# Kernel tuning notes

Measured on AMD Instinct MI355X. Metric: run time of the kernel, lower is better.

Reference implementation:

```python
import jax, jax.numpy as jnp
import numpy as np

N_NODES = 100000


def gcn_conv(x, edge_index, W, b, n_nodes):
    """PyG GCNConv: h = x @ W; add self-loops; symmetric deg norm; sum-aggregate; + bias."""
    src, dst = edge_index[0], edge_index[1]
    loop = jnp.arange(n_nodes, dtype=src.dtype)
    src = jnp.concatenate([src, loop])  # [E + N]
    dst = jnp.concatenate([dst, loop])
    w = jnp.ones(src.shape[0], dtype=x.dtype)  # edge_weight=None -> ones
    deg = jax.ops.segment_sum(w, dst, num_segments=n_nodes)  # in-degree incl. self-loop
    dinv = jnp.where(deg > 0, jax.lax.rsqrt(deg), 0.0).astype(x.dtype)
    norm = dinv[src] * w * dinv[dst]  # [E + N]
    h = x @ W  # [N, d_out] transform first (PyG order)
    msgs = norm[:, None] * h[src]  # [E + N, d_out] gathered, normalized messages
    out = jax.ops.segment_sum(msgs, dst, num_segments=n_nodes)
    return out + b


def setup_inputs() -> dict:
    key = jax.random.key(0)
    k1, k2, k3, k4 = jax.random.split(key, 4)
    d_in, d_hid, d_out = 128, 128, 64
    E = 3200000
    x = jax.random.normal(k1, (N_NODES, d_in), dtype=jnp.float32)
    edge_index = jax.random.randint(k2, (2, E), 0, N_NODES, dtype=jnp.int64)
    W1 = jax.random.normal(k3, (d_in, d_hid), dtype=jnp.float32) / np.sqrt(d_in)
    b1 = jnp.zeros((d_hid,), dtype=jnp.float32)
    W2 = jax.random.normal(k4, (d_hid, d_out), dtype=jnp.float32) / np.sqrt(d_hid)
    b2 = jnp.zeros((d_out,), dtype=jnp.float32)
    return {"x": x, "edge_index": edge_index, "W1": W1, "b1": b1, "W2": W2, "b2": b2}


def reference(x, edge_index, W1, b1, W2, b2):
    h = gcn_conv(x, edge_index, W1, b1, N_NODES)
    h = jax.nn.relu(h)
    out = gcn_conv(h, edge_index, W2, b2, N_NODES)
    return out
```

## Files before the change

### kernel.cpp

```cpp
#include <hip/hip_runtime.h>


#define N_NODES 100000
#define NBLK  512
#define NBUCK 391

typedef __attribute__((ext_vector_type(8))) short short8;
typedef __attribute__((ext_vector_type(4))) float f32x4;

__device__ __forceinline__ unsigned short f2bf(float f) {
    union { float f; unsigned u; } c; c.f = f;
    unsigned r = (c.u + 0x7fffu + ((c.u >> 16) & 1u)) >> 16;
    return (unsigned short)r;
}
__device__ __forceinline__ float2 bfpair(unsigned u) {
    union { float f; unsigned u; } a, b;
    a.u = u << 16; b.u = u & 0xffff0000u;
    return make_float2(a.f, b.f);
}
__device__ __forceinline__ unsigned packbf(float a, float b) {
    return (unsigned)f2bf(a) | ((unsigned)f2bf(b) << 16);
}

__global__ void detect64_k(const unsigned long long* __restrict__ ei, int* __restrict__ flag) {
    unsigned long long v = ei[threadIdx.x & 63];
    unsigned long long bad = __ballot(v >= (1ULL << 32));
    if (threadIdx.x == 0) *flag = (bad == 0ULL) ? 1 : 0;
}

__device__ __forceinline__ int edge_at(const void* ei, int is64, long long idx) {
    if (is64) return (int)((const long long*)ei)[idx];
    return ((const int*)ei)[idx];
}

__global__ __launch_bounds__(256) void count1_k(const void* __restrict__ ei,
                                                const int* __restrict__ flag,
                                                int* __restrict__ bhist, int E) {
    __shared__ int lh[NBUCK];
    int t = threadIdx.x;
    for (int i = t; i < NBUCK; i += 256) lh[i] = 0;
    __syncthreads();
    int is64 = *flag;
    int C = (E + NBLK - 1) / NBLK;
    int lo = blockIdx.x * C;
    int hi = lo + C; if (hi > E) hi = E;
    for (int e = lo + t; e < hi; e += 256) {
        int d = edge_at(ei, is64, (long long)E + e);
        if ((unsigned)d < (unsigned)N_NODES) atomicAdd(&lh[d >> 8], 1);
    }
    __syncthreads();
    for (int i = t; i < NBUCK; i += 256) bhist[(size_t)i * NBLK + blockIdx.x] = lh[i];
}

__global__ void scan1_k(const int* __restrict__ cnt, int* __restrict__ partial,
                        int* __restrict__ bsum, int n) {
    __shared__ int sm[256];
    int t = threadIdx.x;
    int base = blockIdx.x * 1024 + t * 4;
    int v[4]; int loc = 0;
#pragma unroll
    for (int j = 0; j < 4; ++j) { v[j] = (base + j < n) ? cnt[base + j] : 0; loc += v[j]; }
    sm[t] = loc; __syncthreads();
    for (int off = 1; off < 256; off <<= 1) {
        int x = (t >= off) ? sm[t - off] : 0;
        __syncthreads();
        sm[t] += x;
        __syncthreads();
    }
    int incl = sm[t];
    int run = incl - loc;
    if (t == 255) bsum[blockIdx.x] = incl;
#pragma unroll
    for (int j = 0; j < 4; ++j) {
        if (base + j < n) partial[base + j] = run;
        run += v[j];
    }
}

__global__ void scan2_k(int* __restrict__ bsum, int nb) {
    __shared__ int sm[256];
    int t = threadIdx.x;
    int v = (t < nb) ? bsum[t] : 0;
    sm[t] = v; __syncthreads();
    for (int off = 1; off < 256; off <<= 1) {
        int x = (t >= off) ? sm[t - off] : 0;
        __syncthreads();
        sm[t] += x;
        __syncthreads();
    }
    if (t < nb) bsum[t] = sm[t] - v;
}

__global__ void scanadd_k(const int* __restrict__ bsum, int* __restrict__ arr,
                          const int* __restrict__ raw, int* __restrict__ tot, int n) {
    int base = blockIdx.x * 1024 + threadIdx.x * 4;
    int add = bsum[blockIdx.x];
#pragma unroll
    for (int j = 0; j < 4; ++j) {
        int i = base + j;
        if (i < n) {
            int v = arr[i] + add;
            arr[i] = v;
            if (i == n - 1) *tot = v + raw[i];
        }
    }
}

__global__ void scan3_k(const int* __restrict__ bsum, const int* __restrict__ cnt,
                        int* __restrict__ row_ptr, float* __restrict__ dinv, int n) {
    int base = blockIdx.x * 1024 + threadIdx.x * 4;
    int add = bsum[blockIdx.x];
#pragma unroll
    for (int j = 0; j < 4; ++j) {
        int i = base + j;
        if (i < n) {
            row_ptr[i] += add;
            dinv[i] = rsqrtf((float)(cnt[i] + 1));
        }
    }
}

__global__ __launch_bounds__(256) void write1_k(const void* __restrict__ ei,
                                                const int* __restrict__ flag,
                                                const int* __restrict__ bbase,
                                                unsigned* __restrict__ pairs, int E) {
    __shared__ int lofs[NBUCK];
    int t = threadIdx.x;
    for (int i = t; i < NBUCK; i += 256) lofs[i] = bbase[(size_t)i * NBLK + blockIdx.x];
    __syncthreads();
    int is64 = *flag;
    int C = (E + NBLK - 1) / NBLK;
    int lo = blockIdx.x * C;
    int hi = lo + C; if (hi > E) hi = E;
    for (int e = lo + t; e < hi; e += 256) {
        int s = edge_at(ei, is64, e);
        int d = edge_at(ei, is64, (long long)E + e);
        if ((unsigned)d >= (unsigned)N_NODES) continue;
        if ((unsigned)s >= (unsigned)N_NODES) s = 0;
        int b = d >> 8;
        int p = atomicAdd(&lofs[b], 1);
        pairs[p] = (unsigned)s | ((unsigned)(d & 255) << 17);
    }
}

__global__ __launch_bounds__(256) void degree_k(const unsigned* __restrict__ pairs,
                                                const int* __restrict__ bbase,
                                                const int* __restrict__ tot,
                                                int* __restrict__ cnt, int Nn) {
    __shared__ int lh[256];
    int b = blockIdx.x;
    int t = threadIdx.x;
    lh[t] = 0;
    __syncthreads();
    int lo = bbase[(size_t)b * NBLK];
    int hi = (b == NBUCK - 1) ? *tot : bbase[((size_t)b + 1) * NBLK];
    for (int i = lo + t; i < hi; i += 256) {
        unsigned p = __builtin_nontemporal_load(pairs + i);
        atomicAdd(&lh[p >> 17], 1);
    }
    __syncthreads();
    int n0 = b << 8;
    if (n0 + t < Nn) cnt[n0 + t] = lh[t];
}

__global__ __launch_bounds__(256) void fill3_k(const unsigned* __restrict__ pairs,
                                               const int* __restrict__ bbase,
                                               const int* __restrict__ tot,
                                               const int* __restrict__ row_ptr,
                                               int* __restrict__ colv, int Nn) {
    __shared__ int cur[256];
    int b = blockIdx.x;
    int t = threadIdx.x;
    int n0 = b << 8;
    int nn = Nn - n0; if (nn > 256) nn = 256;
    if (t < nn) cur[t] = row_ptr[n0 + t];
    __syncthreads();
    int lo = bbase[(size_t)b * NBLK];
    int hi = (b == NBUCK - 1) ? *tot : bbase[((size_t)b + 1) * NBLK];
    for (int i = lo + t; i < hi; i += 256) {
        unsigned p = __builtin_nontemporal_load(pairs + i);
        int dl = (int)(p >> 17);
        int slot = atomicAdd(&cur[dl], 1);
        colv[slot] = (int)(p & 0x1FFFFu);
    }
}

__global__ void prep_w_k(const float* __restrict__ W1, const float* __restrict__ W2,
                         unsigned short* __restrict__ w1bf, unsigned short* __restrict__ w2bf) {
    int i = blockIdx.x * 256 + threadIdx.x;
    if (i < 128 * 128) { int k = i >> 7, f = i & 127; w1bf[f * 128 + k] = f2bf(W1[i]); }
    if (i < 128 * 64)  { int k = i >> 6, f = i & 63;  w2bf[f * 128 + k] = f2bf(W2[i]); }
}

__global__ __launch_bounds__(256) void gemm1_k(const float* __restrict__ x,
                                               const unsigned short* __restrict__ w1bf,
                                               unsigned* __restrict__ h1, int Nn) {
    __shared__ __align__(16) unsigned short sA[128][136];
    __shared__ __align__(16) unsigned short sB[64][136];
    int tid = threadIdx.x;
    int n0g = blockIdx.x * 64;
    {
        const uint4* src = (const uint4*)w1bf;
#pragma unroll
        for (int l = 0; l < 8; ++l) {
            int idx = tid + l * 256;
            int f = idx >> 4, kq = idx & 15;
            *(uint4*)&sA[f][kq * 8] = src[idx];
        }
    }
    {
        int n = tid >> 2, kq = tid & 3;
        int gn = n0g + n; if (gn >= Nn) gn = Nn - 1;
        const float4* xr = (const float4*)(x + (size_t)gn * 128 + kq * 32);
        unsigned short* dst = &sB[n][kq * 32];
#pragma unroll
        for (int i = 0; i < 8; ++i) {
            float4 v = xr[i];
            dst[i * 4 + 0] = f2bf(v.x); dst[i * 4 + 1] = f2bf(v.y);
            dst[i * 4 + 2] = f2bf(v.z); dst[i * 4 + 3] = f2bf(v.w);
        }
    }
    __syncthreads();
    int wave = tid >> 6, lane = tid & 63;
    int quad = lane >> 4, l16 = lane & 15;
    f32x4 z = {0.f, 0.f, 0.f, 0.f};
    f32x4 acc[8];
#pragma unroll
    for (int t = 0; t < 8; ++t) acc[t] = z;
#pragma unroll
    for (int kk = 0; kk < 4; ++kk) {
        int kb = kk * 32 + quad * 8;
        short8 a = *(const short8*)&sB[wave * 16 + l16][kb];
#pragma unroll
        for (int ft = 0; ft < 8; ++ft) {
            short8 b = *(const short8*)&sA[ft * 16 + l16][kb];
            acc[ft] = __builtin_amdgcn_mfma_f32_16x16x32_bf16(a, b, acc[ft], 0, 0, 0);
        }
    }
    __syncthreads();
    unsigned short (*sC)[136] = sA;
#pragma unroll
    for (int ft = 0; ft < 8; ++ft)
#pragma unroll
        for (int r = 0; r < 4; ++r)
            sC[wave * 16 + quad * 4 + r][ft * 16 + l16] = f2bf(acc[ft][r]);
    __syncthreads();
#pragma unroll
    for (int l = 0; l < 4; ++l) {
        int idx = tid + l * 256;
        int row = idx >> 4, q = idx & 15;
        int gn = n0g + row;
        if (gn < Nn)
            *(uint4*)&h1[(size_t)gn * 64 + q * 4] = *(uint4*)&sC[row][q * 8];
    }
}

__global__ __launch_bounds__(256) void gemm2_k(const unsigned* __restrict__ hr,
                                               const unsigned short* __restrict__ w2bf,
                                               unsigned* __restrict__ h2, int Nn) {
    __shared__ __align__(16) unsigned short sA[64][136];
    __shared__ __align__(16) unsigned short sB[64][136];
    int tid = threadIdx.x;
    int n0g = blockIdx.x * 64;
    {
        const uint4* src = (const uint4*)w2bf;
#pragma unroll
        for (int l = 0; l < 4; ++l) {
            int idx = tid + l * 256;
            int f = idx >> 4, kq = idx & 15;
            *(uint4*)&sA[f][kq * 8] = src[idx];
        }
    }
    {
        const uint4* src = (const uint4*)hr;
#pragma unroll
        for (int l = 0; l < 4; ++l) {
            int idx = tid + l * 256;
            int row = idx >> 4, q = idx & 15;
            int gn = n0g + row; if (gn >= Nn) gn = Nn - 1;
            *(uint4*)&sB[row][q * 8] = src[(size_t)gn * 16 + q];
        }
    }
    __syncthreads();
    int wave = tid >> 6, lane = tid & 63;
    int quad = lane >> 4, l16 = lane & 15;
    f32x4 z = {0.f, 0.f, 0.f, 0.f};
    f32x4 acc[4];
#pragma unroll
    for (int t = 0; t < 4; ++t) acc[t] = z;
#pragma unroll
    for (int kk = 0; kk < 4; ++kk) {
        int kb = kk * 32 + quad * 8;
        short8 a = *(const short8*)&sB[wave * 16 + l16][kb];
#pragma unroll
        for (int ft = 0; ft < 4; ++ft) {
            short8 b = *(const short8*)&sA[ft * 16 + l16][kb];
            acc[ft] = __builtin_amdgcn_mfma_f32_16x16x32_bf16(a, b, acc[ft], 0, 0, 0);
        }
    }
    __syncthreads();
    unsigned short (*sC)[136] = sA;
#pragma unroll
    for (int ft = 0; ft < 4; ++ft)
#pragma unroll
        for (int r = 0; r < 4; ++r)
            sC[wave * 16 + quad * 4 + r][ft * 16 + l16] = f2bf(acc[ft][r]);
    __syncthreads();
#pragma unroll
    for (int l = 0; l < 2; ++l) {
        int idx = tid + l * 256;
        int row = idx >> 3, q = idx & 7;
        int gn = n0g + row;
        if (gn < Nn)
            *(uint4*)&h2[(size_t)gn * 32 + q * 4] = *(uint4*)&sC[row][q * 8];
    }
}

__global__ __launch_bounds__(256) void agg1_k(const unsigned* __restrict__ h,
                                              const int* __restrict__ row_ptr,
                                              const int* __restrict__ cnt,
                                              const int* __restrict__ colv,
                                              const float* __restrict__ dinv,
                                              const float* __restrict__ bias,
                                              unsigned* __restrict__ out, int Nn, int E) {
    int node = blockIdx.x * 4 + (threadIdx.x >> 6);
    if (node >= Nn) return;
    int lane = threadIdx.x & 63;
    float di = dinv[node];
    int start = row_ptr[node];
    int deg = cnt[node];

    float2 hv = bfpair(h[(size_t)node * 64 + lane]);
    float w0 = di * di;
    float ax = w0 * hv.x, ay = w0 * hv.y;

    for (int base = 0; base < deg; base += 64) {
        int idx = base + lane;
        int ci = start + idx; if (ci >= E) ci = E - 1;
        int sl = colv[ci];
        float wl = (idx < deg) ? dinv[sl] : 0.f;
        int m = deg - base; if (m > 64) m = 64;
        int j = 0;
        for (; j + 4 <= m; j += 4) {
            int s0 = __shfl(sl, j),     s1 = __shfl(sl, j + 1);
            int s2 = __shfl(sl, j + 2), s3 = __shfl(sl, j + 3);
            float e0 = di * __shfl(wl, j),     e1 = di * __shfl(wl, j + 1);
            float e2 = di * __shfl(wl, j + 2), e3 = di * __shfl(wl, j + 3);
            unsigned u0 = h[(size_t)s0 * 64 + lane];
            unsigned u1 = h[(size_t)s1 * 64 + lane];
            unsigned u2 = h[(size_t)s2 * 64 + lane];
            unsigned u3 = h[(size_t)s3 * 64 + lane];
            float2 v0 = bfpair(u0), v1 = bfpair(u1), v2 = bfpair(u2), v3 = bfpair(u3);
            ax = fmaf(e0, v0.x, ax); ay = fmaf(e0, v0.y, ay);
            ax = fmaf(e1, v1.x, ax); ay = fmaf(e1, v1.y, ay);
            ax = fmaf(e2, v2.x, ax); ay = fmaf(e2, v2.y, ay);
            ax = fmaf(e3, v3.x, ax); ay = fmaf(e3, v3.y, ay);
        }
        for (; j < m; ++j) {
            int s = __shfl(sl, j);
            float we = di * __shfl(wl, j);
            float2 v = bfpair(h[(size_t)s * 64 + lane]);
            ax = fmaf(we, v.x, ax); ay = fmaf(we, v.y, ay);
        }
    }
    float r0 = fmaxf(ax + bias[lane * 2], 0.f);
    float r1 = fmaxf(ay + bias[lane * 2 + 1], 0.f);
    out[(size_t)node * 64 + lane] = packbf(r0, r1);
}

__global__ __launch_bounds__(256) void agg2_k(const unsigned* __restrict__ h,
                                              const int* __restrict__ row_ptr,
                                              const int* __restrict__ cnt,
                                              const int* __restrict__ colv,
                                              const float* __restrict__ dinv,
                                              const float* __restrict__ bias,
                                              float* __restrict__ out, int Nn, int E) {
    int node = blockIdx.x * 4 + (threadIdx.x >> 6);
    if (node >= Nn) return;
    int lane = threadIdx.x & 63;
    int half = lane >> 5, fp = lane & 31;
    float di = dinv[node];
    int start = row_ptr[node];
    int deg = cnt[node];

    float2 hv = bfpair(h[(size_t)node * 32 + fp]);
    float w0 = (half == 0) ? di * di : 0.f;
    float ax = w0 * hv.x, ay = w0 * hv.y;

    for (int base = 0; base < deg; base += 64) {
        int idx = base + lane;
        int ci = start + idx; if (ci >= E) ci = E - 1;
        int sl = colv[ci];
        float wl = (idx < deg) ? dinv[sl] : 0.f;
        int m = deg - base; if (m > 64) m = 64;
        int j = 0;
        for (; j + 8 <= m; j += 8) {
            int q0 = j + half, q1 = j + 2 + half, q2 = j + 4 + half, q3 = j + 6 + half;
            int s0 = __shfl(sl, q0), s1 = __shfl(sl, q1);
            int s2 = __shfl(sl, q2), s3 = __shfl(sl, q3);
            float e0 = di * __shfl(wl, q0), e1 = di * __shfl(wl, q1);
            float e2 = di * __shfl(wl, q2), e3 = di * __shfl(wl, q3);
            unsigned u0 = h[(size_t)s0 * 32 + fp];
            unsigned u1 = h[(size_t)s1 * 32 + fp];
            unsigned u2 = h[(size_t)s2 * 32 + fp];
            unsigned u3 = h[(size_t)s3 * 32 + fp];
            float2 v0 = bfpair(u0), v1 = bfpair(u1), v2 = bfpair(u2), v3 = bfpair(u3);
            ax = fmaf(e0, v0.x, ax); ay = fmaf(e0, v0.y, ay);
            ax = fmaf(e1, v1.x, ax); ay = fmaf(e1, v1.y, ay);
            ax = fmaf(e2, v2.x, ax); ay = fmaf(e2, v2.y, ay);
            ax = fmaf(e3, v3.x, ax); ay = fmaf(e3, v3.y, ay);
        }
        for (; j < m; j += 2) {
            int q = j + half;
            int s = __shfl(sl, q & 63);
            float we = di * __shfl(wl, q & 63);
            float2 v = bfpair(h[(size_t)s * 32 + fp]);
            ax = fmaf(we, v.x, ax); ay = fmaf(we, v.y, ay);
        }
    }
    ax += __shfl_xor(ax, 32, 64);
    ay += __shfl_xor(ay, 32, 64);
    if (half == 0) {
        float2 r = make_float2(ax + bias[fp * 2], ay + bias[fp * 2 + 1]);
        *(float2*)&out[(size_t)node * 64 + fp * 2] = r;
    }
}

extern "C" void kernel_launch(void* const* d_in, const int* in_sizes, int n_in,
                              void* d_out, int out_size, void* d_ws, size_t ws_size,
                              hipStream_t stream) {
    const float* x  = (const float*)d_in[0];
    const void*  ei = d_in[1];
    const float* W1 = (const float*)d_in[2];
    const float* b1 = (const float*)d_in[3];
    const float* W2 = (const float*)d_in[4];
    const float* b2 = (const float*)d_in[5];

    const int N = N_NODES;
    const int E = in_sizes[1] / 2;
    const int NB = NBLK * NBUCK;

    char* w = (char*)d_ws;
    size_t off = 0;
    auto take = [&](size_t bytes) {
        void* p = w + off;
        off = (off + bytes + 255) & ~(size_t)255;
        return p;
    };
    int*   flag    = (int*)take(2 * sizeof(int));
    int*   tot     = flag + 1;
    int*   cnt     = (int*)take((size_t)N * 4);
    int*   row_ptr = (int*)take((size_t)N * 4);
    int*   bsumA   = (int*)take(256 * 4);
    int*   bsumB   = (int*)take(256 * 4);
    int*   bhist   = (int*)take((size_t)NB * 4);
    int*   bbase   = (int*)take((size_t)NB * 4);
    float* dinv    = (float*)take((size_t)N * 4);
    unsigned* pairs = (unsigned*)take((size_t)E * 4);
    int*   colv    = (int*)take((size_t)E * 4);
    unsigned short* w1bf = (unsigned short*)take(128 * 128 * 2);
    unsigned short* w2bf = (unsigned short*)take(64 * 128 * 2);
    unsigned* hr   = (unsigned*)take((size_t)N * 64 * 4);
    unsigned* h2   = (unsigned*)take((size_t)N * 32 * 4);
    (void)ws_size; (void)n_in; (void)out_size;

    unsigned* h1 = (unsigned*)d_out;

    const int nscanN = (N + 1023) / 1024;
    const int nscanB = (NB + 1023) / 1024;

    detect64_k<<<1, 64, 0, stream>>>((const unsigned long long*)ei, flag);
    count1_k<<<NBLK, 256, 0, stream>>>(ei, flag, bhist, E);
    scan1_k<<<nscanB, 256, 0, stream>>>(bhist, bbase, bsumB, NB);
    scan2_k<<<1, 256, 0, stream>>>(bsumB, nscanB);
    scanadd_k<<<nscanB, 256, 0, stream>>>(bsumB, bbase, bhist, tot, NB);
    write1_k<<<NBLK, 256, 0, stream>>>(ei, flag, bbase, pairs, E);
    degree_k<<<NBUCK, 256, 0, stream>>>(pairs, bbase, tot, cnt, N);
    scan1_k<<<nscanN, 256, 0, stream>>>(cnt, row_ptr, bsumA, N);
    scan2_k<<<1, 256, 0, stream>>>(bsumA, nscanN);
    scan3_k<<<nscanN, 256, 0, stream>>>(bsumA, cnt, row_ptr, dinv, N);
    fill3_k<<<NBUCK, 256, 0, stream>>>(pairs, bbase, tot, row_ptr, colv, N);
    prep_w_k<<<64, 256, 0, stream>>>(W1, W2, w1bf, w2bf);

    gemm1_k<<<(N + 63) / 64, 256, 0, stream>>>(x, w1bf, h1, N);
    agg1_k<<<(N + 3) / 4, 256, 0, stream>>>(h1, row_ptr, cnt, colv, dinv, b1, hr, N, E);
    gemm2_k<<<(N + 63) / 64, 256, 0, stream>>>(hr, w2bf, h2, N);
    agg2_k<<<(N + 3) / 4, 256, 0, stream>>>(h2, row_ptr, cnt, colv, dinv, b2, (float*)d_out, N, E);
}
```

Before: 409.1 us.

## Fold source-side degree normalization into GEMM epilogue and simplify aggregation

Each node's transformed features are pre-scaled by its dinv in the GEMM epilogue. This leaves aggregation as a plain sum of gathered rows followed by one multiply by the destination dinv. The per-edge dinv gathers and per-edge multiplies in both aggregation kernels go away, the gather loops are unrolled wider for more loads in flight, and the colv read and hr store use nontemporal hints. The cost is that the scaled values are rounded to bf16 before summation, which slightly changes rounding behaviour.

```diff
diff --git a/kernel.cpp b/kernel.cpp
--- a/kernel.cpp
+++ b/kernel.cpp
@@ -194,6 +194,7 @@
 
 __global__ __launch_bounds__(256) void gemm1_k(const float* __restrict__ x,
                                                const unsigned short* __restrict__ w1bf,
+                                               const float* __restrict__ dinv,
                                                unsigned* __restrict__ h1, int Nn) {
     __shared__ __align__(16) unsigned short sA[128][136];
     __shared__ __align__(16) unsigned short sB[64][136];
@@ -237,13 +238,20 @@
             acc[ft] = __builtin_amdgcn_mfma_f32_16x16x32_bf16(a, b, acc[ft], 0, 0, 0);
         }
     }
+    float dv[4];
+#pragma unroll
+    for (int r = 0; r < 4; ++r) {
+        int gn = n0g + wave * 16 + quad * 4 + r;
+        if (gn >= Nn) gn = Nn - 1;
+        dv[r] = dinv[gn];
+    }
     __syncthreads();
     unsigned short (*sC)[136] = sA;
 #pragma unroll
     for (int ft = 0; ft < 8; ++ft)
 #pragma unroll
         for (int r = 0; r < 4; ++r)
-            sC[wave * 16 + quad * 4 + r][ft * 16 + l16] = f2bf(acc[ft][r]);
+            sC[wave * 16 + quad * 4 + r][ft * 16 + l16] = f2bf(dv[r] * acc[ft][r]);
     __syncthreads();
 #pragma unroll
     for (int l = 0; l < 4; ++l) {
@@ -257,6 +265,7 @@
 
 __global__ __launch_bounds__(256) void gemm2_k(const unsigned* __restrict__ hr,
                                                const unsigned short* __restrict__ w2bf,
+                                               const float* __restrict__ dinv,
                                                unsigned* __restrict__ h2, int Nn) {
     __shared__ __align__(16) unsigned short sA[64][136];
     __shared__ __align__(16) unsigned short sB[64][136];
@@ -298,13 +307,20 @@
             acc[ft] = __builtin_amdgcn_mfma_f32_16x16x32_bf16(a, b, acc[ft], 0, 0, 0);
         }
     }
+    float dv[4];
+#pragma unroll
+    for (int r = 0; r < 4; ++r) {
+        int gn = n0g + wave * 16 + quad * 4 + r;
+        if (gn >= Nn) gn = Nn - 1;
+        dv[r] = dinv[gn];
+    }
     __syncthreads();
     unsigned short (*sC)[136] = sA;
 #pragma unroll
     for (int ft = 0; ft < 4; ++ft)
 #pragma unroll
         for (int r = 0; r < 4; ++r)
-            sC[wave * 16 + quad * 4 + r][ft * 16 + l16] = f2bf(acc[ft][r]);
+            sC[wave * 16 + quad * 4 + r][ft * 16 + l16] = f2bf(dv[r] * acc[ft][r]);
     __syncthreads();
 #pragma unroll
     for (int l = 0; l < 2; ++l) {
@@ -331,41 +347,52 @@
     int deg = cnt[node];
 
     float2 hv = bfpair(h[(size_t)node * 64 + lane]);
-    float w0 = di * di;
-    float ax = w0 * hv.x, ay = w0 * hv.y;
+    float ax = hv.x, ay = hv.y;
 
     for (int base = 0; base < deg; base += 64) {
         int idx = base + lane;
         int ci = start + idx; if (ci >= E) ci = E - 1;
-        int sl = colv[ci];
-        float wl = (idx < deg) ? dinv[sl] : 0.f;
+        int sl = __builtin_nontemporal_load(colv + ci);
         int m = deg - base; if (m > 64) m = 64;
         int j = 0;
+        for (; j + 8 <= m; j += 8) {
+            int s0 = __shfl(sl, j),     s1 = __shfl(sl, j + 1);
+            int s2 = __shfl(sl, j + 2), s3 = __shfl(sl, j + 3);
+            int s4 = __shfl(sl, j + 4), s5 = __shfl(sl, j + 5);
+            int s6 = __shfl(sl, j + 6), s7 = __shfl(sl, j + 7);
+            unsigned u0 = h[(size_t)s0 * 64 + lane];
+            unsigned u1 = h[(size_t)s1 * 64 + lane];
+            unsigned u2 = h[(size_t)s2 * 64 + lane];
+            unsigned u3 = h[(size_t)s3 * 64 + lane];
+            unsigned u4 = h[(size_t)s4 * 64 + lane];
+            unsigned u5 = h[(size_t)s5 * 64 + lane];
+            unsigned u6 = h[(size_t)s6 * 64 + lane];
+            unsigned u7 = h[(size_t)s7 * 64 + lane];
+            float2 v0 = bfpair(u0), v1 = bfpair(u1), v2 = bfpair(u2), v3 = bfpair(u3);
+            float2 v4 = bfpair(u4), v5 = bfpair(u5), v6 = bfpair(u6), v7 = bfpair(u7);
+            ax += ((v0.x + v1.x) + (v2.x + v3.x)) + ((v4.x + v5.x) + (v6.x + v7.x));
+            ay += ((v0.y + v1.y) + (v2.y + v3.y)) + ((v4.y + v5.y) + (v6.y + v7.y));
+        }
         for (; j + 4 <= m; j += 4) {
             int s0 = __shfl(sl, j),     s1 = __shfl(sl, j + 1);
             int s2 = __shfl(sl, j + 2), s3 = __shfl(sl, j + 3);
-            float e0 = di * __shfl(wl, j),     e1 = di * __shfl(wl, j + 1);
-            float e2 = di * __shfl(wl, j + 2), e3 = di * __shfl(wl, j + 3);
             unsigned u0 = h[(size_t)s0 * 64 + lane];
             unsigned u1 = h[(size_t)s1 * 64 + lane];
             unsigned u2 = h[(size_t)s2 * 64 + lane];
             unsigned u3 = h[(size_t)s3 * 64 + lane];
             float2 v0 = bfpair(u0), v1 = bfpair(u1), v2 = bfpair(u2), v3 = bfpair(u3);
-            ax = fmaf(e0, v0.x, ax); ay = fmaf(e0, v0.y, ay);
-            ax = fmaf(e1, v1.x, ax); ay = fmaf(e1, v1.y, ay);
-            ax = fmaf(e2, v2.x, ax); ay = fmaf(e2, v2.y, ay);
-            ax = fmaf(e3, v3.x, ax); ay = fmaf(e3, v3.y, ay);
+            ax += (v0.x + v1.x) + (v2.x + v3.x);
+            ay += (v0.y + v1.y) + (v2.y + v3.y);
         }
         for (; j < m; ++j) {
             int s = __shfl(sl, j);
-            float we = di * __shfl(wl, j);
             float2 v = bfpair(h[(size_t)s * 64 + lane]);
-            ax = fmaf(we, v.x, ax); ay = fmaf(we, v.y, ay);
-        }
-    }
-    float r0 = fmaxf(ax + bias[lane * 2], 0.f);
-    float r1 = fmaxf(ay + bias[lane * 2 + 1], 0.f);
-    out[(size_t)node * 64 + lane] = packbf(r0, r1);
+            ax += v.x; ay += v.y;
+        }
+    }
+    float r0 = fmaxf(fmaf(di, ax, bias[lane * 2]), 0.f);
+    float r1 = fmaxf(fmaf(di, ay, bias[lane * 2 + 1]), 0.f);
+    __builtin_nontemporal_store(packbf(r0, r1), &out[(size_t)node * 64 + lane]);
 }
 
 __global__ __launch_bounds__(256) void agg2_k(const unsigned* __restrict__ h,
@@ -384,44 +411,59 @@
     int deg = cnt[node];
 
     float2 hv = bfpair(h[(size_t)node * 32 + fp]);
-    float w0 = (half == 0) ? di * di : 0.f;
-    float ax = w0 * hv.x, ay = w0 * hv.y;
+    float ax = (half == 0) ? hv.x : 0.f;
+    float ay = (half == 0) ? hv.y : 0.f;
 
     for (int base = 0; base < deg; base += 64) {
         int idx = base + lane;
         int ci = start + idx; if (ci >= E) ci = E - 1;
-        int sl = colv[ci];
-        float wl = (idx < deg) ? dinv[sl] : 0.f;
+        int sl = __builtin_nontemporal_load(colv + ci);
         int m = deg - base; if (m > 64) m = 64;
         int j = 0;
+        for (; j + 16 <= m; j += 16) {
+            int q0 = j + half,      q1 = j + 2 + half,  q2 = j + 4 + half,  q3 = j + 6 + half;
+            int q4 = j + 8 + half,  q5 = j + 10 + half, q6 = j + 12 + half, q7 = j + 14 + half;
+            int s0 = __shfl(sl, q0), s1 = __shfl(sl, q1);
+            int s2 = __shfl(sl, q2), s3 = __shfl(sl, q3);
+            int s4 = __shfl(sl, q4), s5 = __shfl(sl, q5);
+            int s6 = __shfl(sl, q6), s7 = __shfl(sl, q7);
+            unsigned u0 = h[(size_t)s0 * 32 + fp];
+            unsigned u1 = h[(size_t)s1 * 32 + fp];
+            unsigned u2 = h[(size_t)s2 * 32 + fp];
+            unsigned u3 = h[(size_t)s3 * 32 + fp];
+            unsigned u4 = h[(size_t)s4 * 32 + fp];
+            unsigned u5 = h[(size_t)s5 * 32 + fp];
+            unsigned u6 = h[(size_t)s6 * 32 + fp];
+            unsigned u7 = h[(size_t)s7 * 32 + fp];
+            float2 v0 = bfpair(u0), v1 = bfpair(u1), v2 = bfpair(u2), v3 = bfpair(u3);
+            float2 v4 = bfpair(u4), v5 = bfpair(u5), v6 = bfpair(u6), v7 = bfpair(u7);
+            ax += ((v0.x + v1.x) + (v2.x + v3.x)) + ((v4.x + v5.x) + (v6.x + v7.x));
+            ay += ((v0.y + v1.y) + (v2.y + v3.y)) + ((v4.y + v5.y) + (v6.y + v7.y));
+        }
         for (; j + 8 <= m; j += 8) {
             int q0 = j + half, q1 = j + 2 + half, q2 = j + 4 + half, q3 = j + 6 + half;
             int s0 = __shfl(sl, q0), s1 = __shfl(sl, q1);
             int s2 = __shfl(sl, q2), s3 = __shfl(sl, q3);
-            float e0 = di * __shfl(wl, q0), e1 = di * __shfl(wl, q1);
-            float e2 = di * __shfl(wl, q2), e3 = di * __shfl(wl, q3);
             unsigned u0 = h[(size_t)s0 * 32 + fp];
             unsigned u1 = h[(size_t)s1 * 32 + fp];
             unsigned u2 = h[(size_t)s2 * 32 + fp];
             unsigned u3 = h[(size_t)s3 * 32 + fp];
             float2 v0 = bfpair(u0), v1 = bfpair(u1), v2 = bfpair(u2), v3 = bfpair(u3);
-            ax = fmaf(e0, v0.x, ax); ay = fmaf(e0, v0.y, ay);
-            ax = fmaf(e1, v1.x, ax); ay = fmaf(e1, v1.y, ay);
-            ax = fmaf(e2, v2.x, ax); ay = fmaf(e2, v2.y, ay);
-            ax = fmaf(e3, v3.x, ax); ay = fmaf(e3, v3.y, ay);
+            ax += (v0.x + v1.x) + (v2.x + v3.x);
+            ay += (v0.y + v1.y) + (v2.y + v3.y);
         }
         for (; j < m; j += 2) {
             int q = j + half;
             int s = __shfl(sl, q & 63);
-            float we = di * __shfl(wl, q & 63);
+            float w = (q < m) ? 1.f : 0.f;
             float2 v = bfpair(h[(size_t)s * 32 + fp]);
-            ax = fmaf(we, v.x, ax); ay = fmaf(we, v.y, ay);
+            ax = fmaf(w, v.x, ax); ay = fmaf(w, v.y, ay);
         }
     }
     ax += __shfl_xor(ax, 32, 64);
     ay += __shfl_xor(ay, 32, 64);
     if (half == 0) {
-        float2 r = make_float2(ax + bias[fp * 2], ay + bias[fp * 2 + 1]);
+        float2 r = make_float2(fmaf(di, ax, bias[fp * 2]), fmaf(di, ay, bias[fp * 2 + 1]));
         *(float2*)&out[(size_t)node * 64 + fp * 2] = r;
     }
 }
@@ -482,8 +524,8 @@
     fill3_k<<<NBUCK, 256, 0, stream>>>(pairs, bbase, tot, row_ptr, colv, N);
     prep_w_k<<<64, 256, 0, stream>>>(W1, W2, w1bf, w2bf);
 
-    gemm1_k<<<(N + 63) / 64, 256, 0, stream>>>(x, w1bf, h1, N);
+    gemm1_k<<<(N + 63) / 64, 256, 0, stream>>>(x, w1bf, dinv, h1, N);
     agg1_k<<<(N + 3) / 4, 256, 0, stream>>>(h1, row_ptr, cnt, colv, dinv, b1, hr, N, E);
-    gemm2_k<<<(N + 63) / 64, 256, 0, stream>>>(hr, w2bf, h2, N);
+    gemm2_k<<<(N + 63) / 64, 256, 0, stream>>>(hr, w2bf, dinv, h2, N);
     agg2_k<<<(N + 3) / 4, 256, 0, stream>>>(h2, row_ptr, cnt, colv, dinv, b2, (float*)d_out, N, E);
 }
```

Result: no change. 409.6 us (+0.1%).
